# Optimization experiments

Hardware: AMD Instinct MI355X
Metric: run time of the kernel (lower is better)

The kernel has to match this reference:

```python
import jax, jax.numpy as jnp
import numpy as np

B, C, D, W, H = 2, 256, 16, 32, 32
CS = 256          # in_channels_style
SN = 256          # number of style tokens
HEADS = 8
DH = C // HEADS
EPS = 1e-6


def setup_inputs() -> dict:
    key = jax.random.key(0)
    ks = jax.random.split(key, 8)
    x = jax.random.normal(ks[0], (B, C, D, W, H), dtype=jnp.float32)
    s = jax.random.normal(ks[1], (B, SN, CS), dtype=jnp.float32)
    # learned parameters
    ln_w = jnp.ones((C,), jnp.float32)
    ln_b = jnp.zeros((C,), jnp.float32)
    lns_w = jnp.ones((CS,), jnp.float32)
    lns_b = jnp.zeros((CS,), jnp.float32)
    sc = 0.02
    Wq = jax.random.normal(ks[2], (C, C), jnp.float32) * sc   # (out, in) 1x1 conv3d
    Wk = jax.random.normal(ks[3], (C, CS), jnp.float32) * sc  # Linear weight (out, in)
    Wv = jax.random.normal(ks[4], (C, CS), jnp.float32) * sc
    Wo = jax.random.normal(ks[5], (C, C), jnp.float32) * sc   # proj_out 1x1 conv3d
    bo = jnp.zeros((C,), jnp.float32)
    return {"x": x, "s": s, "ln_w": ln_w, "ln_b": ln_b, "lns_w": lns_w,
            "lns_b": lns_b, "Wq": Wq, "Wk": Wk, "Wv": Wv, "Wo": Wo, "bo": bo}


def reference(x, s, ln_w, ln_b, lns_w, lns_b, Wq, Wk, Wv, Wo, bo):
    b = x.shape[0]
    # channels_first LayerNorm over channel dim (dim 1) of 5D tensor
    u = x.mean(axis=1, keepdims=True)
    var = ((x - u) ** 2).mean(axis=1, keepdims=True)
    hn = (x - u) / jnp.sqrt(var + EPS)
    hn = ln_w[None, :, None, None, None] * hn + ln_b[None, :, None, None, None]
    # standard LayerNorm on last dim of style tokens
    mu = s.mean(axis=-1, keepdims=True)
    sv = ((s - mu) ** 2).mean(axis=-1, keepdims=True)
    sn = (s - mu) / jnp.sqrt(sv + EPS) * lns_w + lns_b
    # projections: 1x1 conv3d == channel matmul; linears on style
    q = jnp.einsum('bcdwh,oc->bodwh', hn, Wq)               # (B,C,D,W,H)
    k = jnp.einsum('bnc,oc->bon', sn, Wk)                    # (B,C,Sn)
    v = jnp.einsum('bnc,oc->bon', sn, Wv)                    # (B,C,Sn)
    d, w, h = q.shape[2], q.shape[3], q.shape[4]
    N = d * w * h
    q = q.reshape(b * HEADS, DH, N).transpose(0, 2, 1)       # (B*h, N, dh)
    k = k.reshape(b * HEADS, DH, SN)                         # (B*h, dh, Sn)
    v = v.reshape(b * HEADS, DH, SN)                         # (B*h, dh, Sn)
    scores = jnp.einsum('bnd,bds->bns', q, k) * (DH ** -0.5)
    attn = jax.nn.softmax(scores, axis=2)                    # (B*h, N, Sn)
    out = jnp.einsum('bds,bns->bdn', v, attn)                # (B*h, dh, N)
    out = out.reshape(b, C, d, w, h)
    out = jnp.einsum('bcdwh,oc->bodwh', out, Wo) + bo[None, :, None, None, None]
    return x + out
```

## Files before the change

### kernel.cpp

```cpp
#include <hip/hip_runtime.h>

#define EPS_ 1e-6f

typedef __attribute__((ext_vector_type(8))) short bf16x8;
typedef __attribute__((ext_vector_type(4))) float f32x4;

__device__ __forceinline__ unsigned short f2b(float f){
  union { float f; unsigned int u; } v; v.f = f;
  unsigned int r = v.u + 0x7fffu + ((v.u >> 16) & 1u);
  return (unsigned short)(r >> 16);
}
__device__ __forceinline__ unsigned int packrne(float a, float b){
  return (unsigned int)f2b(a) | ((unsigned int)f2b(b) << 16);
}
__device__ __forceinline__ unsigned int packtr(float a, float b){
  return (__float_as_uint(a) >> 16) | (__float_as_uint(b) & 0xffff0000u);
}
union cvt8 { unsigned int u[4]; bf16x8 v; };

__global__ __launch_bounds__(256) void k_prep(
    const float* __restrict__ Wq, const float* __restrict__ Wk,
    const float* __restrict__ Wv, const float* __restrict__ Wo,
    const float* __restrict__ s, const float* __restrict__ lns_w,
    const float* __restrict__ lns_b,
    unsigned short* __restrict__ bWq, unsigned short* __restrict__ bWo,
    unsigned short* __restrict__ Kb, unsigned short* __restrict__ Vb){
  __shared__ unsigned short snb[64*264];
  int t = threadIdx.x;
  int blk = blockIdx.x;
  if (blk < 256){
    int i = blk*256 + t;
    bWq[i] = f2b(Wq[i]);
    bWo[i] = f2b(Wo[i]);
    return;
  }
  int idx = blk - 256;
  int b = idx >> 3, n0 = ((idx >> 1) & 3) * 64, mat = idx & 1;
  int tok = t >> 2, sub = t & 3;
  {
    const float4* srow = (const float4*)(s + ((size_t)(b*256 + n0 + tok))*256 + sub*64);
    float4 vv[16];
    float s1 = 0.f, s2 = 0.f;
    #pragma unroll
    for (int j=0;j<16;++j){
      float4 v = srow[j]; vv[j] = v;
      s1 += (v.x+v.y)+(v.z+v.w);
      s2 += (v.x*v.x+v.y*v.y)+(v.z*v.z+v.w*v.w);
    }
    s1 += __shfl_xor(s1,1); s1 += __shfl_xor(s1,2);
    s2 += __shfl_xor(s2,1); s2 += __shfl_xor(s2,2);
    float mu = s1*(1.f/256.f);
    float rstd = rsqrtf(s2*(1.f/256.f) - mu*mu + EPS_);
    const float4* wr = (const float4*)(lns_w + sub*64);
    const float4* br = (const float4*)(lns_b + sub*64);
    #pragma unroll
    for (int j=0;j<16;++j){
      float4 v = vv[j], g = wr[j], o = br[j];
      float n0v = (v.x-mu)*rstd*g.x + o.x;
      float n1v = (v.y-mu)*rstd*g.y + o.y;
      float n2v = (v.z-mu)*rstd*g.z + o.z;
      float n3v = (v.w-mu)*rstd*g.w + o.w;
      uint2 pk = { packrne(n0v,n1v), packrne(n2v,n3v) };
      *(uint2*)&snb[tok*264 + sub*64 + j*4] = pk;
    }
  }
  __syncthreads();
  int lane = t & 63, w = t >> 6, quad = lane >> 4, l16 = lane & 15;
  const float* W = mat ? Wv : Wk;
  f32x4 acc[4][4];
  #pragma unroll
  for (int ot=0;ot<4;++ot)
    #pragma unroll
    for (int nt=0;nt<4;++nt) acc[ot][nt] = (f32x4){0.f,0.f,0.f,0.f};
  for (int ks=0; ks<8; ++ks){
    bf16x8 afr[4], bfr[4];
    #pragma unroll
    for (int ot=0;ot<4;++ot){
      const float4* wr = (const float4*)(W + (size_t)(w*64 + ot*16 + l16)*256 + ks*32 + quad*8);
      float4 a0 = wr[0], a1 = wr[1];
      cvt8 cv;
      cv.u[0]=packrne(a0.x,a0.y); cv.u[1]=packrne(a0.z,a0.w);
      cv.u[2]=packrne(a1.x,a1.y); cv.u[3]=packrne(a1.z,a1.w);
      afr[ot] = cv.v;
    }
    #pragma unroll
    for (int nt=0;nt<4;++nt)
      bfr[nt] = *(const bf16x8*)&snb[(nt*16+l16)*264 + ks*32 + quad*8];
    #pragma unroll
    for (int ot=0;ot<4;++ot)
      #pragma unroll
      for (int nt=0;nt<4;++nt)
        acc[ot][nt] = __builtin_amdgcn_mfma_f32_16x16x32_bf16(afr[ot], bfr[nt], acc[ot][nt], 0,0,0);
  }
  #pragma unroll
  for (int ot=0;ot<4;++ot){
    int otg = w*4 + ot;
    int h = otg >> 1, dbase = (otg&1)*16 + quad*4;
    #pragma unroll
    for (int nt=0;nt<4;++nt){
      int n = n0 + nt*16 + l16;
      if (!mat){
        uint2 pk = { packrne(acc[ot][nt][0], acc[ot][nt][1]),
                     packrne(acc[ot][nt][2], acc[ot][nt][3]) };
        *(uint2*)&Kb[(((size_t)(b*8+h))*256 + n)*32 + dbase] = pk;
      } else {
        #pragma unroll
        for (int r=0;r<4;++r)
          Vb[(((size_t)(b*8+h))*32 + dbase + r)*256 + n] = f2b(acc[ot][nt][r]);
      }
    }
  }
}

__global__ __launch_bounds__(256,2) void k_mega(
    const float* __restrict__ x, const float* __restrict__ ln_w,
    const float* __restrict__ ln_b,
    const unsigned short* __restrict__ bWq, const unsigned short* __restrict__ bWo,
    const unsigned short* __restrict__ Kb, const unsigned short* __restrict__ Vb,
    const float* __restrict__ bo, float* __restrict__ out){
  __shared__ unsigned short buf1[32*264];
  __shared__ float st[512];
  int t = threadIdx.x;
  int blk = blockIdx.x;
  int b = blk >> 9, p0 = (blk & 511) << 5;
  int pp = t & 31, seg = t >> 5;
  const float* xb = x + ((size_t)b << 22) + p0 + pp;

  float s1=0.f, s2=0.f;
  for (int k=0;k<16;++k){
    int c = seg*32 + 2*k;
    float v0 = xb[(size_t)c << 14], v1 = xb[(size_t)(c+1) << 14];
    s1 += v0+v1; s2 += v0*v0+v1*v1;
    *(unsigned int*)&buf1[pp*264 + c] = packrne(v0, v1);
  }
  st[seg*32+pp] = s1; st[256+seg*32+pp] = s2;
  __syncthreads();
  float a=0.f, q=0.f;
  #pragma unroll
  for (int g=0; g<8; ++g){ a += st[g*32+pp]; q += st[256+g*32+pp]; }
  float mu = a*(1.f/256.f);
  float rstd = rsqrtf(q*(1.f/256.f) - mu*mu + EPS_);
  for (int k=0;k<16;++k){
    int c = seg*32 + 2*k;
    unsigned int pk = *(unsigned int*)&buf1[pp*264 + c];
    float v0 = __uint_as_float(pk << 16);
    float v1 = __uint_as_float(pk & 0xffff0000u);
    v0 = (v0-mu)*rstd*ln_w[c]   + ln_b[c];
    v1 = (v1-mu)*rstd*ln_w[c+1] + ln_b[c+1];
    *(unsigned int*)&buf1[pp*264 + c] = packrne(v0, v1);
  }
  __syncthreads();

  int lane = t & 63, w = t >> 6, quad = lane >> 4, l16 = lane & 15;
  int ptile = w & 1, ohalf = w >> 1;
  int prow = ptile*16 + l16;
  const float qs = 0.17677669529663689f * 1.44269504088896341f;

  {
    f32x4 acc[4][2];
    #pragma unroll
    for (int ot=0;ot<4;++ot)
      #pragma unroll
      for (int pt=0;pt<2;++pt) acc[ot][pt] = (f32x4){0.f,0.f,0.f,0.f};
    const unsigned short* wq = bWq + (size_t)(w*64 + l16)*256 + quad*8;
    #pragma unroll 2
    for (int ks=0; ks<8; ++ks){
      bf16x8 bfr[2], afr[4];
      #pragma unroll
      for (int ot=0;ot<4;++ot)
        afr[ot] = *(const bf16x8*)(wq + (size_t)ot*16*256 + ks*32);
      #pragma unroll
      for (int pt=0;pt<2;++pt)
        bfr[pt] = *(const bf16x8*)&buf1[(pt*16+l16)*264 + ks*32 + quad*8];
      #pragma unroll
      for (int ot=0;ot<4;++ot)
        #pragma unroll
        for (int pt=0;pt<2;++pt)
          acc[ot][pt] = __builtin_amdgcn_mfma_f32_16x16x32_bf16(afr[ot], bfr[pt], acc[ot][pt], 0,0,0);
    }
    __syncthreads();
    #pragma unroll
    for (int ot=0;ot<4;++ot){
      int o = w*64 + ot*16 + quad*4;
      #pragma unroll
      for (int pt=0;pt<2;++pt){
        uint2 pk = { packrne(acc[ot][pt][0]*qs, acc[ot][pt][1]*qs),
                     packrne(acc[ot][pt][2]*qs, acc[ot][pt][3]*qs) };
        *(uint2*)&buf1[(pt*16+l16)*264 + o] = pk;
      }
    }
  }
  __syncthreads();

  int srcA = ((( 2*quad   )&3)<<4) + l16;
  int srcB = (((2*quad + 1)&3)<<4) + l16;
  bool hiq = quad >= 2;
  bf16x8 qf[4];
  #pragma unroll
  for (int hh=0;hh<4;++hh)
    qf[hh] = *(const bf16x8*)&buf1[prow*264 + (ohalf*4+hh)*32 + quad*8];

  for (int hh=0; hh<4; ++hh){
    int h = ohalf*4 + hh;
    int bh = b*8 + h;
    const unsigned short* kb = Kb + (size_t)bh*8192 + quad*8;
    const unsigned short* vb = Vb + (size_t)bh*8192 + quad*8;
    f32x4 av[2] = {{0.f,0.f,0.f,0.f},{0.f,0.f,0.f,0.f}};
    float sm0=0.f, sm1=0.f, sm2=0.f, sm3=0.f;
    #pragma unroll 4
    for (int ks=0; ks<8; ++ks){
      bf16x8 kf0 = *(const bf16x8*)(kb + (size_t)((2*ks  )*16+l16)*32);
      bf16x8 kf1 = *(const bf16x8*)(kb + (size_t)((2*ks+1)*16+l16)*32);
      bf16x8 vf0 = *(const bf16x8*)(vb + (size_t)(     l16)*256 + ks*32);
      bf16x8 vf1 = *(const bf16x8*)(vb + (size_t)(16 + l16)*256 + ks*32);
      f32x4 z = {0.f,0.f,0.f,0.f};
      __builtin_amdgcn_s_setprio(1);
      f32x4 s0 = __builtin_amdgcn_mfma_f32_16x16x32_bf16(kf0, qf[hh], z, 0,0,0);
      f32x4 s1 = __builtin_amdgcn_mfma_f32_16x16x32_bf16(kf1, qf[hh], z, 0,0,0);
      __builtin_amdgcn_s_setprio(0);
      float e00 = exp2f(s0[0]), e01 = exp2f(s0[1]);
      float e02 = exp2f(s0[2]), e03 = exp2f(s0[3]);
      float e10 = exp2f(s1[0]), e11 = exp2f(s1[1]);
      float e12 = exp2f(s1[2]), e13 = exp2f(s1[3]);
      sm0 += e00 + e10; sm1 += e01 + e11;
      sm2 += e02 + e12; sm3 += e03 + e13;
      unsigned int p00 = packtr(e00, e01), p01 = packtr(e02, e03);
      unsigned int p10 = packtr(e10, e11), p11 = packtr(e12, e13);
      unsigned int aA0 = (unsigned int)__shfl((int)p00, srcA);
      unsigned int aB0 = (unsigned int)__shfl((int)p10, srcA);
      unsigned int aA1 = (unsigned int)__shfl((int)p01, srcA);
      unsigned int aB1 = (unsigned int)__shfl((int)p11, srcA);
      unsigned int bA0 = (unsigned int)__shfl((int)p00, srcB);
      unsigned int bB0 = (unsigned int)__shfl((int)p10, srcB);
      unsigned int bA1 = (unsigned int)__shfl((int)p01, srcB);
      unsigned int bB1 = (unsigned int)__shfl((int)p11, srcB);
      cvt8 cv;
      cv.u[0] = hiq ? aB0 : aA0;
      cv.u[1] = hiq ? aB1 : aA1;
      cv.u[2] = hiq ? bB0 : bA0;
      cv.u[3] = hiq ? bB1 : bA1;
      bf16x8 pf = cv.v;
      __builtin_amdgcn_s_setprio(1);
      av[0] = __builtin_amdgcn_mfma_f32_16x16x32_bf16(vf0, pf, av[0], 0,0,0);
      av[1] = __builtin_amdgcn_mfma_f32_16x16x32_bf16(vf1, pf, av[1], 0,0,0);
      __builtin_amdgcn_s_setprio(0);
    }
    float sm = (sm0+sm1)+(sm2+sm3);
    sm += __shfl_xor(sm, 16);
    sm += __shfl_xor(sm, 32);
    float inv = 1.f/sm;
    #pragma unroll
    for (int dt=0; dt<2; ++dt){
      uint2 pko = { packrne(av[dt][0]*inv, av[dt][1]*inv),
                    packrne(av[dt][2]*inv, av[dt][3]*inv) };
      *(uint2*)&buf1[prow*264 + h*32 + dt*16 + quad*4] = pko;
    }
  }
  __syncthreads();

  {
    f32x4 oacc[4][2];
    #pragma unroll
    for (int ot=0;ot<4;++ot)
      #pragma unroll
      for (int pt=0;pt<2;++pt) oacc[ot][pt] = (f32x4){0.f,0.f,0.f,0.f};
    const unsigned short* wo = bWo + (size_t)(w*64 + l16)*256 + quad*8;
    #pragma unroll 2
    for (int ks=0; ks<8; ++ks){
      bf16x8 bfr[2], afr[4];
      #pragma unroll
      for (int ot=0;ot<4;++ot)
        afr[ot] = *(const bf16x8*)(wo + (size_t)ot*16*256 + ks*32);
      #pragma unroll
      for (int pt=0;pt<2;++pt)
        bfr[pt] = *(const bf16x8*)&buf1[(pt*16+l16)*264 + ks*32 + quad*8];
      #pragma unroll
      for (int ot=0;ot<4;++ot)
        #pragma unroll
        for (int pt=0;pt<2;++pt)
          oacc[ot][pt] = __builtin_amdgcn_mfma_f32_16x16x32_bf16(afr[ot], bfr[pt], oacc[ot][pt], 0,0,0);
    }
    #pragma unroll
    for (int ot=0;ot<4;++ot){
      int o = w*64 + ot*16 + quad*4;
      #pragma unroll
      for (int pt=0;pt<2;++pt){
        int p = p0 + pt*16 + l16;
        #pragma unroll
        for (int r=0;r<4;++r){
          size_t idx = (((size_t)b*256 + o + r) << 14) + p;
          out[idx] = oacc[ot][pt][r] + bo[o+r] + x[idx];
        }
      }
    }
  }
}

extern "C" void kernel_launch(void* const* d_in, const int* in_sizes, int n_in,
                              void* d_out, int out_size, void* d_ws, size_t ws_size,
                              hipStream_t stream) {
  const float* x     = (const float*)d_in[0];
  const float* s     = (const float*)d_in[1];
  const float* ln_w  = (const float*)d_in[2];
  const float* ln_b  = (const float*)d_in[3];
  const float* lns_w = (const float*)d_in[4];
  const float* lns_b = (const float*)d_in[5];
  const float* Wq    = (const float*)d_in[6];
  const float* Wk    = (const float*)d_in[7];
  const float* Wv    = (const float*)d_in[8];
  const float* Wo    = (const float*)d_in[9];
  const float* bo    = (const float*)d_in[10];
  float* out = (float*)d_out;

  unsigned short* bWq = (unsigned short*)d_ws;
  unsigned short* bWo = bWq + 65536;
  unsigned short* Kb  = bWo + 65536;
  unsigned short* Vb  = Kb + 131072;

  k_prep<<<272,  256, 0, stream>>>(Wq, Wk, Wv, Wo, s, lns_w, lns_b, bWq, bWo, Kb, Vb);
  k_mega<<<1024, 256, 0, stream>>>(x, ln_w, ln_b, bWq, bWo, Kb, Vb, bo, out);
}
```

Baseline: 188.4 us.

## Vectorize LayerNorm x loads, batch residual loads, raise occupancy bound

Restructures the LayerNorm prologue so each thread loads float4 vectors of x across 8 channels, reduces sums with wave shuffles plus a small shared stage, and writes normalized bf16 rows directly, dropping the scalar strided loads and the second LDS pass. The epilogue prefetches all residual x values into registers before writing outputs, so the loads can overlap. The launch bound is raised to 4 blocks per SM, which caps registers per thread and risks spills given the extra vr/xr register arrays.

```diff
diff --git a/kernel.cpp b/kernel.cpp
--- a/kernel.cpp
+++ b/kernel.cpp
@@ -112,7 +112,7 @@
   }
 }
 
-__global__ __launch_bounds__(256,2) void k_mega(
+__global__ __launch_bounds__(256,4) void k_mega(
     const float* __restrict__ x, const float* __restrict__ ln_w,
     const float* __restrict__ ln_b,
     const unsigned short* __restrict__ bWq, const unsigned short* __restrict__ bWo,
@@ -123,31 +123,69 @@
   int t = threadIdx.x;
   int blk = blockIdx.x;
   int b = blk >> 9, p0 = (blk & 511) << 5;
-  int pp = t & 31, seg = t >> 5;
-  const float* xb = x + ((size_t)b << 22) + p0 + pp;
-
-  float s1=0.f, s2=0.f;
-  for (int k=0;k<16;++k){
-    int c = seg*32 + 2*k;
-    float v0 = xb[(size_t)c << 14], v1 = xb[(size_t)(c+1) << 14];
-    s1 += v0+v1; s2 += v0*v0+v1*v1;
-    *(unsigned int*)&buf1[pp*264 + c] = packrne(v0, v1);
-  }
-  st[seg*32+pp] = s1; st[256+seg*32+pp] = s2;
-  __syncthreads();
-  float a=0.f, q=0.f;
-  #pragma unroll
-  for (int g=0; g<8; ++g){ a += st[g*32+pp]; q += st[256+g*32+pp]; }
-  float mu = a*(1.f/256.f);
-  float rstd = rsqrtf(q*(1.f/256.f) - mu*mu + EPS_);
-  for (int k=0;k<16;++k){
-    int c = seg*32 + 2*k;
-    unsigned int pk = *(unsigned int*)&buf1[pp*264 + c];
-    float v0 = __uint_as_float(pk << 16);
-    float v1 = __uint_as_float(pk & 0xffff0000u);
-    v0 = (v0-mu)*rstd*ln_w[c]   + ln_b[c];
-    v1 = (v1-mu)*rstd*ln_w[c+1] + ln_b[c+1];
-    *(unsigned int*)&buf1[pp*264 + c] = packrne(v0, v1);
+
+  {
+    int p4 = t & 7, cg = t >> 3;
+    const float* xq = x + ((size_t)(b*256 + cg*8) << 14) + p0 + p4*4;
+    float vr[8][4];
+    #pragma unroll
+    for (int j=0;j<8;++j){
+      float4 v = *(const float4*)(xq + ((size_t)j << 14));
+      vr[j][0]=v.x; vr[j][1]=v.y; vr[j][2]=v.z; vr[j][3]=v.w;
+    }
+    float s1v[4]={0.f,0.f,0.f,0.f}, s2v[4]={0.f,0.f,0.f,0.f};
+    #pragma unroll
+    for (int j=0;j<8;++j)
+      #pragma unroll
+      for (int i=0;i<4;++i){ s1v[i]+=vr[j][i]; s2v[i]+=vr[j][i]*vr[j][i]; }
+    #pragma unroll
+    for (int i=0;i<4;++i){
+      s1v[i]+=__shfl_xor(s1v[i],8);  s2v[i]+=__shfl_xor(s2v[i],8);
+      s1v[i]+=__shfl_xor(s1v[i],16); s2v[i]+=__shfl_xor(s2v[i],16);
+      s1v[i]+=__shfl_xor(s1v[i],32); s2v[i]+=__shfl_xor(s2v[i],32);
+    }
+    int wv = t >> 6;
+    if ((t & 56) == 0){
+      #pragma unroll
+      for (int i=0;i<4;++i){
+        st[(wv*8 + p4)*4 + i]       = s1v[i];
+        st[128 + (wv*8 + p4)*4 + i] = s2v[i];
+      }
+    }
+    __syncthreads();
+    float mu[4], rstd[4];
+    #pragma unroll
+    for (int i=0;i<4;++i){
+      float a = st[(0*8+p4)*4+i] + st[(1*8+p4)*4+i]
+              + st[(2*8+p4)*4+i] + st[(3*8+p4)*4+i];
+      float q = st[128+(0*8+p4)*4+i] + st[128+(1*8+p4)*4+i]
+              + st[128+(2*8+p4)*4+i] + st[128+(3*8+p4)*4+i];
+      mu[i] = a*(1.f/256.f);
+      rstd[i] = rsqrtf(q*(1.f/256.f) - mu[i]*mu[i] + EPS_);
+    }
+    float lwv[8], lbv[8];
+    {
+      float4 a0 = *(const float4*)(ln_w + cg*8);
+      float4 a1 = *(const float4*)(ln_w + cg*8 + 4);
+      float4 b0 = *(const float4*)(ln_b + cg*8);
+      float4 b1 = *(const float4*)(ln_b + cg*8 + 4);
+      lwv[0]=a0.x; lwv[1]=a0.y; lwv[2]=a0.z; lwv[3]=a0.w;
+      lwv[4]=a1.x; lwv[5]=a1.y; lwv[6]=a1.z; lwv[7]=a1.w;
+      lbv[0]=b0.x; lbv[1]=b0.y; lbv[2]=b0.z; lbv[3]=b0.w;
+      lbv[4]=b1.x; lbv[5]=b1.y; lbv[6]=b1.z; lbv[7]=b1.w;
+    }
+    #pragma unroll
+    for (int i=0;i<4;++i){
+      int prow = p4*4 + i;
+      float n_[8];
+      #pragma unroll
+      for (int j=0;j<8;++j)
+        n_[j] = (vr[j][i]-mu[i])*rstd[i]*lwv[j] + lbv[j];
+      uint2 w0 = { packrne(n_[0],n_[1]), packrne(n_[2],n_[3]) };
+      uint2 w1 = { packrne(n_[4],n_[5]), packrne(n_[6],n_[7]) };
+      *(uint2*)&buf1[prow*264 + cg*8]     = w0;
+      *(uint2*)&buf1[prow*264 + cg*8 + 4] = w1;
+    }
   }
   __syncthreads();
 
@@ -280,6 +318,7 @@
         for (int pt=0;pt<2;++pt)
           oacc[ot][pt] = __builtin_amdgcn_mfma_f32_16x16x32_bf16(afr[ot], bfr[pt], oacc[ot][pt], 0,0,0);
     }
+    float xr[4][2][4];
     #pragma unroll
     for (int ot=0;ot<4;++ot){
       int o = w*64 + ot*16 + quad*4;
@@ -287,9 +326,20 @@
       for (int pt=0;pt<2;++pt){
         int p = p0 + pt*16 + l16;
         #pragma unroll
+        for (int r=0;r<4;++r)
+          xr[ot][pt][r] = x[(((size_t)b*256 + o + r) << 14) + p];
+      }
+    }
+    #pragma unroll
+    for (int ot=0;ot<4;++ot){
+      int o = w*64 + ot*16 + quad*4;
+      #pragma unroll
+      for (int pt=0;pt<2;++pt){
+        int p = p0 + pt*16 + l16;
+        #pragma unroll
         for (int r=0;r<4;++r){
           size_t idx = (((size_t)b*256 + o + r) << 14) + p;
-          out[idx] = oacc[ot][pt][r] + bo[o+r] + x[idx];
+          out[idx] = oacc[ot][pt][r] + bo[o+r] + xr[ot][pt][r];
         }
       }
     }
```

After: 188.6 us. No clear change (+0.1%).
